# Optimization experiments

Measured on AMD Instinct MI355X. Metric: run time of the kernel, lower is better.

The kernel has to match this reference:

```python
import jax, jax.numpy as jnp
import numpy as np

N = 50000
F_IN = 256
H1, D1 = 8, 8            # conv1: 8 heads x 8 dims, concat -> 64
H2, C = 8, 16            # conv2: 8 heads x num_classes, concat -> 128
NEG_SLOPE = 0.2


def setup_inputs() -> dict:
    key = jax.random.key(0)
    ks = jax.random.split(key, 10)
    x = jax.random.normal(ks[0], (N, F_IN), dtype=jnp.float32)
    edge_index = jax.random.randint(ks[1], (2, 800000), 0, N, dtype=jnp.int64)
    s1 = 1.0 / np.sqrt(F_IN)
    s2 = 1.0 / np.sqrt(H1 * D1)
    return {
        "x": x,
        "edge_index": edge_index,
        "W1": jax.random.normal(ks[2], (F_IN, H1 * D1), dtype=jnp.float32) * s1,
        "a1_src": jax.random.normal(ks[3], (H1, D1), dtype=jnp.float32) * s2,
        "a1_dst": jax.random.normal(ks[4], (H1, D1), dtype=jnp.float32) * s2,
        "b1": jnp.zeros((H1 * D1,), dtype=jnp.float32),
        "W2": jax.random.normal(ks[5], (H1 * D1, H2 * C), dtype=jnp.float32) * s2,
        "a2_src": jax.random.normal(ks[6], (H2, C), dtype=jnp.float32) * (1.0 / np.sqrt(C)),
        "a2_dst": jax.random.normal(ks[7], (H2, C), dtype=jnp.float32) * (1.0 / np.sqrt(C)),
        "b2": jnp.zeros((H2 * C,), dtype=jnp.float32),
    }


def _add_self_loops(edge_index, n):
    loops = jnp.arange(n, dtype=edge_index.dtype)
    return jnp.concatenate([edge_index, jnp.stack([loops, loops])], axis=1)


def _gat_conv(x, src, dst, W, a_src, a_dst, b, heads, out_dim, n):
    # xw: [N, H, O]
    xw = (x @ W).reshape(n, heads, out_dim)
    al_src = jnp.einsum("nho,ho->nh", xw, a_src)  # [N, H]
    al_dst = jnp.einsum("nho,ho->nh", xw, a_dst)
    e = jax.nn.leaky_relu(al_src[src] + al_dst[dst], NEG_SLOPE)  # [E, H]
    # segment softmax over edges sharing a destination node
    e_max = jax.ops.segment_max(e, dst, num_segments=n)
    e_exp = jnp.exp(e - e_max[dst])
    denom = jax.ops.segment_sum(e_exp, dst, num_segments=n)
    alpha = e_exp / (denom[dst] + 1e-16)                          # [E, H]
    msg = xw[src] * alpha[:, :, None]                              # [E, H, O]
    out = jax.ops.segment_sum(msg, dst, num_segments=n)           # [N, H, O]
    return out.reshape(n, heads * out_dim) + b, alpha


def reference(x, edge_index, W1, a1_src, a1_dst, b1, W2, a2_src, a2_dst, b2):
    ei = _add_self_loops(edge_index, N)
    src, dst = ei[0], ei[1]
    # dropout is a no-op at inference (training=False)
    h1, alpha1 = _gat_conv(x, src, dst, W1, a1_src, a1_dst, b1, H1, D1, N)
    h1 = jax.nn.elu(h1)
    h2, _ = _gat_conv(h1, src, dst, W2, a2_src, a2_dst, b2, H2, C, N)
    logp = jax.nn.log_softmax(h2, axis=1)
    return logp, alpha1
```

## Files before the change

kernel.cpp:

```cpp
#include <hip/hip_runtime.h>

#define N_NODES 50000
#define N_EDGES 800000
#define N_TOT   850000
#define NEG 0.2f
#define ELLW 64

#define G1_TILES 782
#define G2_TILES 782

#define NBIN   250
#define NPBIN  200
#define BKBLK  200
#define EPBK   4000
#define BCAP   32
#define OCAP   4096

__device__ __forceinline__ float leaky(float x) { return x > 0.f ? x : NEG * x; }

__device__ __forceinline__ unsigned bf16pk(float a, float b) {
  unsigned ua = __float_as_uint(a), ub = __float_as_uint(b);
  ua = (ua + 0x7FFFu + ((ua >> 16) & 1u)) >> 16;
  ub = (ub + 0x7FFFu + ((ub >> 16) & 1u)) >> 16;
  return ua | (ub << 16);
}
__device__ __forceinline__ float blo(unsigned u) { return __uint_as_float(u << 16); }
__device__ __forceinline__ float bhi(unsigned u) { return __uint_as_float(u & 0xFFFF0000u); }
__device__ __forceinline__ float bh2f(unsigned short h) { return __uint_as_float(((unsigned)h) << 16); }

__global__ __launch_bounds__(256) void bin_gemm1_k(const float* __restrict__ x,
    const float* __restrict__ W1, const float* __restrict__ a1sv, const float* __restrict__ a1dv,
    unsigned short* __restrict__ xw1h, float* __restrict__ al1s, float* __restrict__ a1dd,
    const int* __restrict__ srcA, const int* __restrict__ dstA,
    unsigned* __restrict__ slots, unsigned short* __restrict__ bcnt2,
    unsigned* __restrict__ ofl, int* __restrict__ ofc)
{
  __shared__ __align__(16) char smem[33024];
  const int t = threadIdx.x;
  if (blockIdx.x < BKBLK) {
    unsigned (*buf)[BCAP] = (unsigned(*)[BCAP])smem;
    int* bc = (int*)(smem + 32000);
    for (int k = t; k < NBIN; k += 256) bc[k] = 0;
    __syncthreads();
    const int e0 = blockIdx.x * EPBK;
#pragma unroll
    for (int j = 0; j < 4; ++j) {
      int i4 = j * 256 + t;
      if (i4 < EPBK / 4) {
        int4 s4 = ((const int4*)(srcA + e0))[i4];
        int4 d4 = ((const int4*)(dstA + e0))[i4];
        int dd[4] = {d4.x, d4.y, d4.z, d4.w};
        int ss[4] = {s4.x, s4.y, s4.z, s4.w};
#pragma unroll
        for (int q = 0; q < 4; ++q) {
          int bin = dd[q] / NPBIN;
          unsigned rec = (unsigned)dd[q] | ((unsigned)ss[q] << 16);
          int p = atomicAdd(&bc[bin], 1);
          if (p < BCAP) buf[bin][p] = rec;
          else { int g = atomicAdd(ofc, 1); if (g < OCAP) ofl[g] = rec; }
        }
      }
    }
    __syncthreads();
    const int wv = t >> 6, ln = t & 63;
    for (int b = wv; b < NBIN; b += 4) {
      int c = bc[b]; if (c > BCAP) c = BCAP;
      if (ln == 0) bcnt2[(size_t)b * BKBLK + blockIdx.x] = (unsigned short)c;
      if (ln < c) slots[((size_t)b * BKBLK + blockIdx.x) * BCAP + ln] = buf[b][ln];
    }
    return;
  }
  float* xs  = (float*)smem;
  float* wsm = (float*)(smem + 8192);
  const int tx = t & 15, ty = t >> 4;
  const int n0 = (blockIdx.x - BKBLK) * 64;
  const int nl = t >> 2;
  const int ks = (t & 3) * 8;
  const int wk = t >> 3;
  const int wc = (t & 7) * 8;
  int gn = n0 + nl; if (gn >= N_NODES) gn = N_NODES - 1;
  const float* xrowb = x + (size_t)gn * 256 + ks;

  float acc[4][4];
#pragma unroll
  for (int r = 0; r < 4; ++r)
#pragma unroll
    for (int i = 0; i < 4; ++i) acc[r][i] = 0.f;

  float4 xv0, xv1, wv0, wv1;
  {
    const float4* xp = (const float4*)xrowb;
    xv0 = xp[0]; xv1 = xp[1];
    const float* wrow = W1 + (size_t)wk * 64 + wc;
    wv0 = ((const float4*)wrow)[0];
    wv1 = ((const float4*)wrow)[1];
  }
  for (int kc = 0; kc < 8; ++kc) {
    __syncthreads();
    xs[(ks + 0) * 64 + nl] = xv0.x;  xs[(ks + 1) * 64 + nl] = xv0.y;
    xs[(ks + 2) * 64 + nl] = xv0.z;  xs[(ks + 3) * 64 + nl] = xv0.w;
    xs[(ks + 4) * 64 + nl] = xv1.x;  xs[(ks + 5) * 64 + nl] = xv1.y;
    xs[(ks + 6) * 64 + nl] = xv1.z;  xs[(ks + 7) * 64 + nl] = xv1.w;
    ((float4*)&wsm[wk * 64 + wc])[0] = wv0;
    ((float4*)&wsm[wk * 64 + wc])[1] = wv1;
    __syncthreads();
    if (kc < 7) {
      const int kb = (kc + 1) * 32;
      const float4* xp = (const float4*)(xrowb + kb);
      xv0 = xp[0]; xv1 = xp[1];
      const float* wrow = W1 + (size_t)(kb + wk) * 64 + wc;
      wv0 = ((const float4*)wrow)[0];
      wv1 = ((const float4*)wrow)[1];
    }
#pragma unroll 4
    for (int k = 0; k < 32; ++k) {
      float4 xa = *(const float4*)&xs[k * 64 + ty * 4];
      float4 wv = *(const float4*)&wsm[k * 64 + tx * 4];
      float xn[4]; *(float4*)xn = xa;
      float wn[4]; *(float4*)wn = wv;
#pragma unroll
      for (int r = 0; r < 4; ++r)
#pragma unroll
        for (int i = 0; i < 4; ++i) acc[r][i] += xn[r] * wn[i];
    }
  }
  float cs[4], cd[4];
#pragma unroll
  for (int i = 0; i < 4; ++i) { cs[i] = a1sv[tx * 4 + i]; cd[i] = a1dv[tx * 4 + i]; }
#pragma unroll
  for (int r = 0; r < 4; ++r) {
    int n = n0 + ty * 4 + r;
    if (n >= N_NODES) break;
    uint2 pk;
    pk.x = bf16pk(acc[r][0], acc[r][1]);
    pk.y = bf16pk(acc[r][2], acc[r][3]);
    *(uint2*)(xw1h + (size_t)n * 64 + tx * 4) = pk;
    float ps = acc[r][0] * cs[0] + acc[r][1] * cs[1] + acc[r][2] * cs[2] + acc[r][3] * cs[3];
    float pd = acc[r][0] * cd[0] + acc[r][1] * cd[1] + acc[r][2] * cd[2] + acc[r][3] * cd[3];
    ps += __shfl_xor(ps, 1);
    pd += __shfl_xor(pd, 1);
    if ((tx & 1) == 0) {
      al1s[n * 8 + (tx >> 1)] = ps;
      a1dd[n * 16 + (tx >> 1)] = pd;
    }
  }
}

__global__ __launch_bounds__(256) void ell_k(const unsigned* __restrict__ slots,
    const unsigned short* __restrict__ bcnt2, const unsigned* __restrict__ ofl,
    const int* __restrict__ ofc, int* __restrict__ cnt, unsigned short* __restrict__ ell)
{
  __shared__ unsigned short ell_lds[NPBIN * ELLW];
  __shared__ int cnt_lds[NPBIN];
  const int t = threadIdx.x;
  const int b = blockIdx.x;
  for (int k = t; k < NPBIN; k += 256) cnt_lds[k] = 0;
  __syncthreads();
  if (t < BKBLK) {
    int c = bcnt2[(size_t)b * BKBLK + t];
    const uint4* sp4 = (const uint4*)(slots + ((size_t)b * BKBLK + t) * BCAP);
    uint4 R[8];
#pragma unroll
    for (int q = 0; q < 8; ++q) R[q] = sp4[q];
#pragma unroll
    for (int j = 0; j < BCAP; ++j) {
      if (j < c) {
        unsigned rec = ((const unsigned*)R)[j];
        int row = (int)(rec & 0xFFFFu) - b * NPBIN;
        int p = atomicAdd(&cnt_lds[row], 1);
        if (p < ELLW) ell_lds[row * ELLW + p] = (unsigned short)(rec >> 16);
      }
    }
  }
  __syncthreads();
  int oc = *ofc; if (oc > OCAP) oc = OCAP;
  for (int i = t; i < oc; i += 256) {
    unsigned rec = ofl[i];
    int d = rec & 0xFFFFu;
    if (d >= b * NPBIN && d < (b + 1) * NPBIN) {
      int p = atomicAdd(&cnt_lds[d - b * NPBIN], 1);
      if (p < ELLW) ell_lds[(d - b * NPBIN) * ELLW + p] = (unsigned short)(rec >> 16);
    }
  }
  __syncthreads();
  const uint4* s4 = (const uint4*)ell_lds;
  uint4* d4 = (uint4*)(ell + (size_t)b * NPBIN * ELLW);
  for (int i = t; i < NPBIN * ELLW / 8; i += 256) d4[i] = s4[i];
  for (int k = t; k < NPBIN; k += 256) cnt[b * NPBIN + k] = cnt_lds[k];
}

__global__ __launch_bounds__(256) void agg1_k(const unsigned short* __restrict__ xw1h,
    const float* __restrict__ al1s, float* __restrict__ a1dd,
    const int* __restrict__ cnt, const unsigned short* __restrict__ ell,
    const float* __restrict__ b1, float* __restrict__ h1)
{
  const int lane = threadIdx.x & 63;
  const int n = blockIdx.x * 4 + (threadIdx.x >> 6);
  if (n >= N_NODES) return;
  const int h = lane >> 3;
  const int hw = lane & 7;
  const int ew = lane >> 3;
  const float ad = a1dd[n * 16 + h];
  const float adH = __shfl(ad, hw << 3);
  float ws = __expf(leaky(al1s[n * 8 + h] + ad));
  float den0 = ws, den1 = 0.f;
  float acc0 = ws * bh2f(xw1h[(size_t)n * 64 + lane]), acc1 = 0.f;
  int num = cnt[n]; if (num > ELLW) num = ELLW;
  const unsigned short* erow = ell + (size_t)n * ELLW;
  int i = 0;
  for (; i + 8 <= num; i += 8) {
    int sw = erow[i + ew];
    float wv = __expf(leaky(al1s[sw * 8 + hw] + adH));
#pragma unroll
    for (int j = 0; j < 8; ++j) {
      int sj = __shfl(sw, j << 3);
      float wj = __shfl(wv, (j << 3) + h);
      float vj = bh2f(xw1h[(size_t)sj * 64 + lane]);
      if (j & 1) { acc1 += wj * vj; den1 += wj; }
      else       { acc0 += wj * vj; den0 += wj; }
    }
  }
  for (; i < num; ++i) {
    int s = erow[i];
    float w = __expf(leaky(al1s[s * 8 + h] + ad));
    acc0 += w * bh2f(xw1h[(size_t)s * 64 + lane]);
    den0 += w;
  }
  float den = den0 + den1, acc = acc0 + acc1;
  if ((lane & 7) == 0) a1dd[n * 16 + 8 + h] = den;
  float o = acc / (den + 1e-16f) + b1[lane];
  h1[(size_t)n * 64 + lane] = o > 0.f ? o : (__expf(o) - 1.f);
}

__global__ __launch_bounds__(256) void gemm2_alpha_k(const float* __restrict__ h1,
    const float* __restrict__ W2, const float* __restrict__ a2sv, const float* __restrict__ a2dv,
    unsigned* __restrict__ xw2b, float* __restrict__ al2s, float* __restrict__ al2d,
    const int* __restrict__ srcA, const int* __restrict__ dstA,
    const float* __restrict__ al1s, const float* __restrict__ a1dd,
    float* __restrict__ alpha_out)
{
  __shared__ float xs[64 * 64];
  __shared__ float wsm[64 * 128];
  if (blockIdx.x >= G2_TILES) {
    int e = (blockIdx.x - G2_TILES) * 256 + threadIdx.x;
    if (e >= N_TOT) return;
    int s, d;
    if (e < N_EDGES) { s = srcA[e]; d = dstA[e]; }
    else             { s = d = e - N_EDGES; }
    float4 as0 = ((const float4*)(al1s + s * 8))[0];
    float4 as1 = ((const float4*)(al1s + s * 8))[1];
    const float4* dd = (const float4*)(a1dd + d * 16);
    float4 ad0 = dd[0];
    float4 ad1 = dd[1];
    float4 dn0 = dd[2];
    float4 dn1 = dd[3];
    float4 o0, o1;
    o0.x = __expf(leaky(as0.x + ad0.x)) / (dn0.x + 1e-16f);
    o0.y = __expf(leaky(as0.y + ad0.y)) / (dn0.y + 1e-16f);
    o0.z = __expf(leaky(as0.z + ad0.z)) / (dn0.z + 1e-16f);
    o0.w = __expf(leaky(as0.w + ad0.w)) / (dn0.w + 1e-16f);
    o1.x = __expf(leaky(as1.x + ad1.x)) / (dn1.x + 1e-16f);
    o1.y = __expf(leaky(as1.y + ad1.y)) / (dn1.y + 1e-16f);
    o1.z = __expf(leaky(as1.z + ad1.z)) / (dn1.z + 1e-16f);
    o1.w = __expf(leaky(as1.w + ad1.w)) / (dn1.w + 1e-16f);
    ((float4*)(alpha_out + (size_t)e * 8))[0] = o0;
    ((float4*)(alpha_out + (size_t)e * 8))[1] = o1;
    return;
  }
  const int t = threadIdx.x;
  const int tx = t & 15, ty = t >> 4;
  const int n0 = blockIdx.x * 64;
  {
    const int nl = t >> 2;
    const int ks = (t & 3) * 16;
    int gn = n0 + nl; if (gn >= N_NODES) gn = N_NODES - 1;
    const float4* hp = (const float4*)(h1 + (size_t)gn * 64 + ks);
#pragma unroll
    for (int j = 0; j < 4; ++j) {
      float4 v = hp[j];
      xs[(ks + 4 * j + 0) * 64 + nl] = v.x;
      xs[(ks + 4 * j + 1) * 64 + nl] = v.y;
      xs[(ks + 4 * j + 2) * 64 + nl] = v.z;
      xs[(ks + 4 * j + 3) * 64 + nl] = v.w;
    }
    const int wk = t >> 2;
    const int wc = (t & 3) * 32;
    const float4* wp = (const float4*)(W2 + (size_t)wk * 128 + wc);
    float4* wd = (float4*)&wsm[wk * 128 + wc];
#pragma unroll
    for (int j = 0; j < 8; ++j) wd[j] = wp[j];
  }
  __syncthreads();
  float acc[4][8];
#pragma unroll
  for (int r = 0; r < 4; ++r)
#pragma unroll
    for (int i = 0; i < 8; ++i) acc[r][i] = 0.f;
#pragma unroll 4
  for (int k = 0; k < 64; ++k) {
    float4 xa = *(const float4*)&xs[k * 64 + ty * 4];
    float4 wa = *(const float4*)&wsm[k * 128 + tx * 8];
    float4 wb = *(const float4*)&wsm[k * 128 + tx * 8 + 4];
    float xn[4]; *(float4*)xn = xa;
    float wn[8]; *(float4*)&wn[0] = wa; *(float4*)&wn[4] = wb;
#pragma unroll
    for (int r = 0; r < 4; ++r)
#pragma unroll
      for (int i = 0; i < 8; ++i) acc[r][i] += xn[r] * wn[i];
  }
  float cs[8], cd[8];
#pragma unroll
  for (int i = 0; i < 8; ++i) { cs[i] = a2sv[tx * 8 + i]; cd[i] = a2dv[tx * 8 + i]; }
#pragma unroll
  for (int r = 0; r < 4; ++r) {
    int n = n0 + ty * 4 + r;
    if (n >= N_NODES) break;
    uint4 pk;
    pk.x = bf16pk(acc[r][0], acc[r][1]);
    pk.y = bf16pk(acc[r][2], acc[r][3]);
    pk.z = bf16pk(acc[r][4], acc[r][5]);
    pk.w = bf16pk(acc[r][6], acc[r][7]);
    *(uint4*)(xw2b + (size_t)n * 64 + tx * 4) = pk;
    float ps = 0.f, pd = 0.f;
#pragma unroll
    for (int i = 0; i < 8; ++i) { ps += acc[r][i] * cs[i]; pd += acc[r][i] * cd[i]; }
    ps += __shfl_xor(ps, 1);
    pd += __shfl_xor(pd, 1);
    if ((tx & 1) == 0) {
      al2s[n * 8 + (tx >> 1)] = ps;
      al2d[n * 8 + (tx >> 1)] = pd;
    }
  }
}

__global__ __launch_bounds__(256) void agg2_k(const unsigned* __restrict__ xw2b,
    const float* __restrict__ al2s, const float* __restrict__ al2d,
    const int* __restrict__ cnt, const unsigned short* __restrict__ ell,
    const float* __restrict__ b2, float* __restrict__ logp)
{
  const int lane = threadIdx.x & 63;
  const int n = blockIdx.x * 4 + (threadIdx.x >> 6);
  if (n >= N_NODES) return;
  const int h = lane >> 3;
  const int hw = lane & 7;
  const int ew = lane >> 3;
  const float ad = al2d[n * 8 + h];
  const float adH = __shfl(ad, hw << 3);
  float ws = __expf(leaky(al2s[n * 8 + h] + ad));
  unsigned su = xw2b[(size_t)n * 64 + lane];
  float den0 = ws, den1 = 0.f;
  float ax0 = ws * blo(su), ay0 = ws * bhi(su), ax1 = 0.f, ay1 = 0.f;
  int num = cnt[n]; if (num > ELLW) num = ELLW;
  const unsigned short* erow = ell + (size_t)n * ELLW;
  int i = 0;
  for (; i + 8 <= num; i += 8) {
    int sw = erow[i + ew];
    float wv = __expf(leaky(al2s[sw * 8 + hw] + adH));
#pragma unroll
    for (int j = 0; j < 8; ++j) {
      int sj = __shfl(sw, j << 3);
      float wj = __shfl(wv, (j << 3) + h);
      unsigned u = xw2b[(size_t)sj * 64 + lane];
      if (j & 1) { ax1 += wj * blo(u); ay1 += wj * bhi(u); den1 += wj; }
      else       { ax0 += wj * blo(u); ay0 += wj * bhi(u); den0 += wj; }
    }
  }
  for (; i < num; ++i) {
    int s = erow[i];
    float w = __expf(leaky(al2s[s * 8 + h] + ad));
    unsigned u = xw2b[(size_t)s * 64 + lane];
    ax0 += w * blo(u); ay0 += w * bhi(u); den0 += w;
  }
  float inv = 1.f / (den0 + den1 + 1e-16f);
  float o0 = (ax0 + ax1) * inv + b2[2 * lane];
  float o1 = (ay0 + ay1) * inv + b2[2 * lane + 1];
  float mx = fmaxf(o0, o1);
#pragma unroll
  for (int off = 1; off < 64; off <<= 1) mx = fmaxf(mx, __shfl_xor(mx, off));
  float se = __expf(o0 - mx) + __expf(o1 - mx);
#pragma unroll
  for (int off = 1; off < 64; off <<= 1) se += __shfl_xor(se, off);
  float lse = mx + __logf(se);
  float2 o; o.x = o0 - lse; o.y = o1 - lse;
  ((float2*)logp)[(size_t)n * 64 + lane] = o;
}

extern "C" void kernel_launch(void* const* d_in, const int* in_sizes, int n_in,
                              void* d_out, int out_size, void* d_ws, size_t ws_size,
                              hipStream_t stream)
{
  const float* x   = (const float*)d_in[0];
  const int*   ei  = (const int*)d_in[1];
  const float* W1  = (const float*)d_in[2];
  const float* a1s = (const float*)d_in[3];
  const float* a1d = (const float*)d_in[4];
  const float* b1  = (const float*)d_in[5];
  const float* W2  = (const float*)d_in[6];
  const float* a2s = (const float*)d_in[7];
  const float* a2d = (const float*)d_in[8];
  const float* b2  = (const float*)d_in[9];
  const int* srcA = ei;
  const int* dstA = ei + N_EDGES;

  char* ws = (char*)d_ws;
  unsigned short* xw1h = (unsigned short*)ws;            ws += (size_t)N_NODES * 64 * 2;
  float* h1    = (float*)ws;  ws += (size_t)N_NODES * 64 * 4;
  unsigned* xw2b = (unsigned*)ws; ws += (size_t)N_NODES * 64 * 4;
  float* al1s_ = (float*)ws;  ws += (size_t)N_NODES * 8 * 4;
  float* a1dd_ = (float*)ws;  ws += (size_t)N_NODES * 16 * 4;
  float* al2s_ = (float*)ws;  ws += (size_t)N_NODES * 8 * 4;
  float* al2d_ = (float*)ws;  ws += (size_t)N_NODES * 8 * 4;
  int* cnt    = (int*)ws;     ws += (size_t)N_NODES * 4;
  unsigned short* ell = (unsigned short*)ws; ws += (size_t)N_NODES * ELLW * 2;
  unsigned* slots = (unsigned*)ws; ws += (size_t)NBIN * BKBLK * BCAP * 4;
  unsigned short* bcnt2 = (unsigned short*)ws; ws += (size_t)NBIN * BKBLK * 2;
  unsigned* ofl = (unsigned*)ws; ws += (size_t)OCAP * 4;
  int* ofc = (int*)ws; ws += 16;

  float* logp      = (float*)d_out;
  float* alpha_out = logp + (size_t)N_NODES * 128;

  hipMemsetAsync(ofc, 0, sizeof(int), stream);

  bin_gemm1_k<<<BKBLK + G1_TILES, 256, 0, stream>>>(
      x, W1, a1s, a1d, xw1h, al1s_, a1dd_, srcA, dstA, slots, bcnt2, ofl, ofc);
  ell_k<<<NBIN, 256, 0, stream>>>(slots, bcnt2, ofl, ofc, cnt, ell);
  agg1_k<<<(N_NODES + 3) / 4, 256, 0, stream>>>(xw1h, al1s_, a1dd_, cnt, ell, b1, h1);
  gemm2_alpha_k<<<G2_TILES + (N_TOT + 255) / 256, 256, 0, stream>>>(
      h1, W2, a2s, a2d, xw2b, al2s_, al2d_, srcA, dstA, al1s_, a1dd_, alpha_out);
  agg2_k<<<(N_NODES + 3) / 4, 256, 0, stream>>>(xw2b, al2s_, al2d_, cnt, ell, b2, logp);
}
```

Measured before the change: 172.0 us.

## Split wavefront into two half-waves processing alternate edges in aggregation kernels

```diff
diff --git a/kernel.cpp b/kernel.cpp
--- a/kernel.cpp
+++ b/kernel.cpp
@@ -16,7 +16,7 @@
 #define BCAP   32
 #define OCAP   4096
 
-__device__ __forceinline__ float leaky(float x) { return x > 0.f ? x : NEG * x; }
+__device__ __forceinline__ float leaky(float x) { return fmaxf(x, NEG * x); }
 
 __device__ __forceinline__ unsigned bf16pk(float a, float b) {
   unsigned ua = __float_as_uint(a), ub = __float_as_uint(b);
@@ -194,42 +194,65 @@
     const int* __restrict__ cnt, const unsigned short* __restrict__ ell,
     const float* __restrict__ b1, float* __restrict__ h1)
 {
-  const int lane = threadIdx.x & 63;
+  const unsigned lane = threadIdx.x & 63;
   const int n = blockIdx.x * 4 + (threadIdx.x >> 6);
   if (n >= N_NODES) return;
-  const int h = lane >> 3;
-  const int hw = lane & 7;
-  const int ew = lane >> 3;
-  const float ad = a1dd[n * 16 + h];
-  const float adH = __shfl(ad, hw << 3);
-  float ws = __expf(leaky(al1s[n * 8 + h] + ad));
-  float den0 = ws, den1 = 0.f;
-  float acc0 = ws * bh2f(xw1h[(size_t)n * 64 + lane]), acc1 = 0.f;
+  const unsigned sub = lane >> 5;
+  const unsigned c = lane & 31;
+  const unsigned hh = c >> 2;
+  const float ad = a1dd[n * 16 + hh];
+  const unsigned* xv32 = (const unsigned*)xw1h;
+  float ax = 0.f, ay = 0.f, den = 0.f;
+  if (sub == 0) {
+    float ws = __expf(leaky(al1s[n * 8 + hh] + ad));
+    unsigned u = xv32[((unsigned)n << 5) | c];
+    ax = ws * blo(u); ay = ws * bhi(u); den = ws;
+  }
   int num = cnt[n]; if (num > ELLW) num = ELLW;
-  const unsigned short* erow = ell + (size_t)n * ELLW;
+  const uint4* cp = (const uint4*)(ell + (size_t)n * ELLW);
   int i = 0;
   for (; i + 8 <= num; i += 8) {
-    int sw = erow[i + ew];
-    float wv = __expf(leaky(al1s[sw * 8 + hw] + adH));
-#pragma unroll
-    for (int j = 0; j < 8; ++j) {
-      int sj = __shfl(sw, j << 3);
-      float wj = __shfl(wv, (j << 3) + h);
-      float vj = bh2f(xw1h[(size_t)sj * 64 + lane]);
-      if (j & 1) { acc1 += wj * vj; den1 += wj; }
-      else       { acc0 += wj * vj; den0 += wj; }
-    }
-  }
-  for (; i < num; ++i) {
-    int s = erow[i];
-    float w = __expf(leaky(al1s[s * 8 + h] + ad));
-    acc0 += w * bh2f(xw1h[(size_t)s * 64 + lane]);
-    den0 += w;
-  }
-  float den = den0 + den1, acc = acc0 + acc1;
-  if ((lane & 7) == 0) a1dd[n * 16 + 8 + h] = den;
-  float o = acc / (den + 1e-16f) + b1[lane];
-  h1[(size_t)n * 64 + lane] = o > 0.f ? o : (__expf(o) - 1.f);
+    uint4 A = cp[i >> 3];
+    unsigned s0 = sub ? (A.x >> 16) : (A.x & 0xFFFFu);
+    unsigned s1 = sub ? (A.y >> 16) : (A.y & 0xFFFFu);
+    unsigned s2 = sub ? (A.z >> 16) : (A.z & 0xFFFFu);
+    unsigned s3 = sub ? (A.w >> 16) : (A.w & 0xFFFFu);
+    float l0 = al1s[(s0 << 3) + hh], l1 = al1s[(s1 << 3) + hh];
+    float l2 = al1s[(s2 << 3) + hh], l3 = al1s[(s3 << 3) + hh];
+    unsigned u0 = xv32[(s0 << 5) | c], u1 = xv32[(s1 << 5) | c];
+    unsigned u2 = xv32[(s2 << 5) | c], u3 = xv32[(s3 << 5) | c];
+    float w0 = __expf(leaky(l0 + ad)), w1 = __expf(leaky(l1 + ad));
+    float w2 = __expf(leaky(l2 + ad)), w3 = __expf(leaky(l3 + ad));
+    ax += w0 * blo(u0); ay += w0 * bhi(u0);
+    ax += w1 * blo(u1); ay += w1 * bhi(u1);
+    ax += w2 * blo(u2); ay += w2 * bhi(u2);
+    ax += w3 * blo(u3); ay += w3 * bhi(u3);
+    den += w0 + w1 + w2 + w3;
+  }
+  for (; i + 2 <= num; i += 2) {
+    unsigned pr = *(const unsigned*)(ell + (size_t)n * ELLW + i);
+    unsigned s = sub ? (pr >> 16) : (pr & 0xFFFFu);
+    float w = __expf(leaky(al1s[(s << 3) + hh] + ad));
+    unsigned u = xv32[(s << 5) | c];
+    ax += w * blo(u); ay += w * bhi(u); den += w;
+  }
+  if (i < num && sub == 0) {
+    unsigned s = ell[(size_t)n * ELLW + i];
+    float w = __expf(leaky(al1s[(s << 3) + hh] + ad));
+    unsigned u = xv32[(s << 5) | c];
+    ax += w * blo(u); ay += w * bhi(u); den += w;
+  }
+  ax += __shfl_xor(ax, 32); ay += __shfl_xor(ay, 32); den += __shfl_xor(den, 32);
+  if (sub == 0) {
+    if ((c & 3) == 0) a1dd[n * 16 + 8 + hh] = den;
+    float inv = 1.f / (den + 1e-16f);
+    float2 bb = *(const float2*)(b1 + 2 * c);
+    float o0 = ax * inv + bb.x, o1 = ay * inv + bb.y;
+    float2 o;
+    o.x = o0 > 0.f ? o0 : (__expf(o0) - 1.f);
+    o.y = o1 > 0.f ? o1 : (__expf(o1) - 1.f);
+    ((float2*)(h1 + (size_t)n * 64))[c] = o;
+  }
 }
 
 __global__ __launch_bounds__(256) void gemm2_alpha_k(const float* __restrict__ h1,
@@ -338,51 +361,84 @@
     const int* __restrict__ cnt, const unsigned short* __restrict__ ell,
     const float* __restrict__ b2, float* __restrict__ logp)
 {
-  const int lane = threadIdx.x & 63;
+  const unsigned lane = threadIdx.x & 63;
   const int n = blockIdx.x * 4 + (threadIdx.x >> 6);
   if (n >= N_NODES) return;
-  const int h = lane >> 3;
-  const int hw = lane & 7;
-  const int ew = lane >> 3;
-  const float ad = al2d[n * 8 + h];
-  const float adH = __shfl(ad, hw << 3);
-  float ws = __expf(leaky(al2s[n * 8 + h] + ad));
-  unsigned su = xw2b[(size_t)n * 64 + lane];
-  float den0 = ws, den1 = 0.f;
-  float ax0 = ws * blo(su), ay0 = ws * bhi(su), ax1 = 0.f, ay1 = 0.f;
+  const unsigned sub = lane >> 5;
+  const unsigned c = lane & 31;
+  const unsigned hh = c >> 2;
+  const float ad = al2d[n * 8 + hh];
+  const uint2* xv2 = (const uint2*)xw2b;
+  float ax0 = 0.f, ay0 = 0.f, ax1 = 0.f, ay1 = 0.f, den = 0.f;
+  if (sub == 0) {
+    float ws = __expf(leaky(al2s[n * 8 + hh] + ad));
+    uint2 su = xv2[((unsigned)n << 5) | c];
+    ax0 = ws * blo(su.x); ay0 = ws * bhi(su.x);
+    ax1 = ws * blo(su.y); ay1 = ws * bhi(su.y);
+    den = ws;
+  }
   int num = cnt[n]; if (num > ELLW) num = ELLW;
-  const unsigned short* erow = ell + (size_t)n * ELLW;
+  const uint4* cp = (const uint4*)(ell + (size_t)n * ELLW);
   int i = 0;
   for (; i + 8 <= num; i += 8) {
-    int sw = erow[i + ew];
-    float wv = __expf(leaky(al2s[sw * 8 + hw] + adH));
-#pragma unroll
-    for (int j = 0; j < 8; ++j) {
-      int sj = __shfl(sw, j << 3);
-      float wj = __shfl(wv, (j << 3) + h);
-      unsigned u = xw2b[(size_t)sj * 64 + lane];
-      if (j & 1) { ax1 += wj * blo(u); ay1 += wj * bhi(u); den1 += wj; }
-      else       { ax0 += wj * blo(u); ay0 += wj * bhi(u); den0 += wj; }
-    }
-  }
-  for (; i < num; ++i) {
-    int s = erow[i];
-    float w = __expf(leaky(al2s[s * 8 + h] + ad));
-    unsigned u = xw2b[(size_t)s * 64 + lane];
-    ax0 += w * blo(u); ay0 += w * bhi(u); den0 += w;
-  }
-  float inv = 1.f / (den0 + den1 + 1e-16f);
-  float o0 = (ax0 + ax1) * inv + b2[2 * lane];
-  float o1 = (ay0 + ay1) * inv + b2[2 * lane + 1];
-  float mx = fmaxf(o0, o1);
-#pragma unroll
-  for (int off = 1; off < 64; off <<= 1) mx = fmaxf(mx, __shfl_xor(mx, off));
-  float se = __expf(o0 - mx) + __expf(o1 - mx);
-#pragma unroll
-  for (int off = 1; off < 64; off <<= 1) se += __shfl_xor(se, off);
+    uint4 A = cp[i >> 3];
+    unsigned s0 = sub ? (A.x >> 16) : (A.x & 0xFFFFu);
+    unsigned s1 = sub ? (A.y >> 16) : (A.y & 0xFFFFu);
+    unsigned s2 = sub ? (A.z >> 16) : (A.z & 0xFFFFu);
+    unsigned s3 = sub ? (A.w >> 16) : (A.w & 0xFFFFu);
+    float l0 = al2s[(s0 << 3) + hh], l1 = al2s[(s1 << 3) + hh];
+    float l2 = al2s[(s2 << 3) + hh], l3 = al2s[(s3 << 3) + hh];
+    uint2 u0 = xv2[(s0 << 5) | c], u1 = xv2[(s1 << 5) | c];
+    uint2 u2 = xv2[(s2 << 5) | c], u3 = xv2[(s3 << 5) | c];
+    float w0 = __expf(leaky(l0 + ad)), w1 = __expf(leaky(l1 + ad));
+    float w2 = __expf(leaky(l2 + ad)), w3 = __expf(leaky(l3 + ad));
+    ax0 += w0 * blo(u0.x); ay0 += w0 * bhi(u0.x);
+    ax1 += w0 * blo(u0.y); ay1 += w0 * bhi(u0.y);
+    ax0 += w1 * blo(u1.x); ay0 += w1 * bhi(u1.x);
+    ax1 += w1 * blo(u1.y); ay1 += w1 * bhi(u1.y);
+    ax0 += w2 * blo(u2.x); ay0 += w2 * bhi(u2.x);
+    ax1 += w2 * blo(u2.y); ay1 += w2 * bhi(u2.y);
+    ax0 += w3 * blo(u3.x); ay0 += w3 * bhi(u3.x);
+    ax1 += w3 * blo(u3.y); ay1 += w3 * bhi(u3.y);
+    den += w0 + w1 + w2 + w3;
+  }
+  for (; i + 2 <= num; i += 2) {
+    unsigned pr = *(const unsigned*)(ell + (size_t)n * ELLW + i);
+    unsigned s = sub ? (pr >> 16) : (pr & 0xFFFFu);
+    float w = __expf(leaky(al2s[(s << 3) + hh] + ad));
+    uint2 u = xv2[(s << 5) | c];
+    ax0 += w * blo(u.x); ay0 += w * bhi(u.x);
+    ax1 += w * blo(u.y); ay1 += w * bhi(u.y);
+    den += w;
+  }
+  if (i < num && sub == 0) {
+    unsigned s = ell[(size_t)n * ELLW + i];
+    float w = __expf(leaky(al2s[(s << 3) + hh] + ad));
+    uint2 u = xv2[(s << 5) | c];
+    ax0 += w * blo(u.x); ay0 += w * bhi(u.x);
+    ax1 += w * blo(u.y); ay1 += w * bhi(u.y);
+    den += w;
+  }
+  ax0 += __shfl_xor(ax0, 32); ay0 += __shfl_xor(ay0, 32);
+  ax1 += __shfl_xor(ax1, 32); ay1 += __shfl_xor(ay1, 32);
+  den += __shfl_xor(den, 32);
+  float inv = 1.f / (den + 1e-16f);
+  float4 bb = *(const float4*)(b2 + 4 * c);
+  float o0 = ax0 * inv + bb.x;
+  float o1 = ay0 * inv + bb.y;
+  float o2 = ax1 * inv + bb.z;
+  float o3 = ay1 * inv + bb.w;
+  float mx = fmaxf(fmaxf(o0, o1), fmaxf(o2, o3));
+#pragma unroll
+  for (int off = 1; off < 32; off <<= 1) mx = fmaxf(mx, __shfl_xor(mx, off));
+  float se = __expf(o0 - mx) + __expf(o1 - mx) + __expf(o2 - mx) + __expf(o3 - mx);
+#pragma unroll
+  for (int off = 1; off < 32; off <<= 1) se += __shfl_xor(se, off);
   float lse = mx + __logf(se);
-  float2 o; o.x = o0 - lse; o.y = o1 - lse;
-  ((float2*)logp)[(size_t)n * 64 + lane] = o;
+  if (sub == 0) {
+    float4 o; o.x = o0 - lse; o.y = o1 - lse; o.z = o2 - lse; o.w = o3 - lse;
+    ((float4*)(logp + (size_t)n * 128))[c] = o;
+  }
 }
 
 extern "C" void kernel_launch(void* const* d_in, const int* in_sizes, int n_in,
```

New measurement: 159.6 us. -7.2%, faster.
